# Optimization experiments

Hardware: AMD Instinct MI355X
Metric: run time of the kernel (lower is better)

Reference implementation:

```python
import jax, jax.numpy as jnp
import numpy as np


def setup_inputs() -> dict:
    key = jax.random.key(0)
    k1, k2 = jax.random.split(key)
    B, T_enc, T_dec, D = 8, 2048, 2048, 128
    encoder_hidden_states = jax.random.normal(k1, (B, T_enc, D), dtype=jnp.float32)
    decoder_hidden_states = jax.random.normal(k2, (B, T_dec, D), dtype=jnp.float32)
    return {"encoder_hidden_states": encoder_hidden_states,
            "decoder_hidden_states": decoder_hidden_states}


def reference(encoder_hidden_states, decoder_hidden_states):
    # dot_product[b,q,k] = dec[b,q,:] . enc[b,k,:]
    dot_product = jnp.einsum("bqd,bkd->bqk", decoder_hidden_states, encoder_hidden_states)
    # attn_scores[b,q,d] = sum_k dot_product[b,q,k] * enc[b,k,d]
    # (the torch code materializes the 4D broadcast; this is the same math as a bmm)
    attn_scores = jnp.einsum("bqk,bkd->bqd", dot_product, encoder_hidden_states)
    return attn_scores
```

## Files before the change

### kernel.cpp

```cpp
#include <hip/hip_runtime.h>

#define BB 8
#define TT 2048
#define DD 128
#define CH 32
#define GT_STRIDE 72

typedef __attribute__((ext_vector_type(8))) short bf16x8;
typedef __attribute__((ext_vector_type(4))) float f32x4;
typedef unsigned short u16;

static __device__ __forceinline__ float bf2f(u16 u) {
    union { unsigned int i; float f; } v; v.i = ((unsigned int)u) << 16; return v.f;
}
static __device__ __forceinline__ u16 f2bf(float f) {
    union { float f; unsigned int i; } v; v.f = f;
    unsigned int x = v.i;
    return (u16)((x + 0x7FFFu + ((x >> 16) & 1u)) >> 16);
}

__global__ __launch_bounds__(256, 1) void gram_mfma(const float* __restrict__ enc,
                                                    u16* __restrict__ P) {
    const int b     = blockIdx.y;
    const int chunk = blockIdx.x;
    const int t     = threadIdx.x;

    __shared__ __align__(16) u16 Gt[DD * GT_STRIDE];

    const int d  = t & 127;
    const int kh = t >> 7;
    const int wave = t >> 6, lane = t & 63, quad = lane >> 4, ln = lane & 15;

    f32x4 acc[2][8];
    #pragma unroll
    for (int mi = 0; mi < 2; ++mi)
        #pragma unroll
        for (int nt = 0; nt < 8; ++nt) acc[mi][nt] = (f32x4){0.f, 0.f, 0.f, 0.f};

    const float* src = enc + ((size_t)b * TT + (size_t)chunk * 64) * DD;
    #pragma unroll
    for (int a = 0; a < 8; ++a) {
        const int k4 = a * 2 + kh;
        u16 o[4];
        #pragma unroll
        for (int i = 0; i < 4; ++i)
            o[i] = f2bf(src[(k4 * 4 + i) * DD + d]);
        *(ushort4*)&Gt[d * GT_STRIDE + k4 * 4] = *(const ushort4*)o;
    }
    __syncthreads();

    bf16x8 afrag[2][2];
    #pragma unroll
    for (int mi = 0; mi < 2; ++mi)
        #pragma unroll
        for (int ks = 0; ks < 2; ++ks)
            afrag[mi][ks] = *(const bf16x8*)&Gt[((wave * 2 + mi) * 16 + ln) * GT_STRIDE
                                                + ks * 32 + quad * 8];
    #pragma unroll
    for (int ks = 0; ks < 2; ++ks) {
        #pragma unroll
        for (int nt = 0; nt < 8; ++nt) {
            const bf16x8 bfrag = *(const bf16x8*)&Gt[(nt * 16 + ln) * GT_STRIDE
                                                     + ks * 32 + quad * 8];
            #pragma unroll
            for (int mi = 0; mi < 2; ++mi)
                acc[mi][nt] = __builtin_amdgcn_mfma_f32_16x16x32_bf16(
                    afrag[mi][ks], bfrag, acc[mi][nt], 0, 0, 0);
        }
    }

    u16* Pb = P + ((size_t)chunk * BB + b) * (DD * DD);
    const int off = ln * 16 + (quad >> 1) * 8 + (quad & 1) * 4;
    #pragma unroll
    for (int mi = 0; mi < 2; ++mi) {
        #pragma unroll
        for (int nt = 0; nt < 8; ++nt) {
            u16 o[4];
            #pragma unroll
            for (int r = 0; r < 4; ++r) o[r] = f2bf(acc[mi][nt][r]);
            const int tile = (wave * 2 + mi) * 8 + nt;
            *(ushort4*)&Pb[tile * 256 + off] = *(const ushort4*)o;
        }
    }
}

__global__ __launch_bounds__(128) void gram_reduce(const u16* __restrict__ P,
                                                   u16* __restrict__ Gw) {
    const int g = blockIdx.x * 128 + threadIdx.x;
    const ushort4* Pu = (const ushort4*)P;
    const int stride = BB * DD * DD / 4;
    float sx = 0.f, sy = 0.f, sz = 0.f, sw = 0.f;
    #pragma unroll
    for (int c = 0; c < CH; ++c) {
        const ushort4 v = Pu[(size_t)c * stride + g];
        sx += bf2f(v.x); sy += bf2f(v.y); sz += bf2f(v.z); sw += bf2f(v.w);
    }
    ushort4 o; o.x = f2bf(sx); o.y = f2bf(sy); o.z = f2bf(sz); o.w = f2bf(sw);
    ((ushort4*)Gw)[g] = o;
}

__global__ __launch_bounds__(256, 1) void apply_mfma(const float* __restrict__ dec,
                                                     const u16* __restrict__ Gw,
                                                     float* __restrict__ out) {
    const int b     = blockIdx.y;
    const int chunk = blockIdx.x;
    const int t     = threadIdx.x;

    __shared__ __align__(16) u16 Gs[DD * DD];

    const int wave = t >> 6, lane = t & 63, quad = lane >> 4, ln = lane & 15;
    const int qt = wave * 16;

    const float* drow = dec + ((size_t)b * TT + (size_t)chunk * 64 + qt + ln) * DD
                        + quad * 8;
    float4 dv[4][2];
    #pragma unroll
    for (int ks = 0; ks < 4; ++ks) {
        dv[ks][0] = *(const float4*)(drow + ks * 32);
        dv[ks][1] = *(const float4*)(drow + ks * 32 + 4);
    }

    const uint4* gsrc = (const uint4*)(Gw + (size_t)b * DD * DD);
    #pragma unroll
    for (int i = 0; i < 8; ++i)
        ((uint4*)Gs)[i * 256 + t] = gsrc[i * 256 + t];

    bf16x8 afrag[4];
    #pragma unroll
    for (int ks = 0; ks < 4; ++ks) {
        union { u16 o[8]; bf16x8 v; } u;
        u.o[0] = f2bf(dv[ks][0].x); u.o[1] = f2bf(dv[ks][0].y);
        u.o[2] = f2bf(dv[ks][0].z); u.o[3] = f2bf(dv[ks][0].w);
        u.o[4] = f2bf(dv[ks][1].x); u.o[5] = f2bf(dv[ks][1].y);
        u.o[6] = f2bf(dv[ks][1].z); u.o[7] = f2bf(dv[ks][1].w);
        afrag[ks] = u.v;
    }
    __syncthreads();

    f32x4 acc[8];
    #pragma unroll
    for (int dt = 0; dt < 8; ++dt) acc[dt] = (f32x4){0.f, 0.f, 0.f, 0.f};

    #pragma unroll
    for (int ks = 0; ks < 4; ++ks) {
        const int mtk  = ks * 2 + (quad >> 1);
        const int boff = ln * 16 + (quad & 1) * 8;
        #pragma unroll
        for (int dt = 0; dt < 8; ++dt) {
            const bf16x8 bb = *(const bf16x8*)&Gs[(mtk * 8 + dt) * 256 + boff];
            acc[dt] = __builtin_amdgcn_mfma_f32_16x16x32_bf16(afrag[ks], bb, acc[dt], 0, 0, 0);
        }
    }

    float* ob = out + ((size_t)b * TT + (size_t)chunk * 64) * DD;
    #pragma unroll
    for (int dt = 0; dt < 8; ++dt) {
        const int dcol = dt * 16 + ln;
        #pragma unroll
        for (int r = 0; r < 4; ++r) {
            const int q = qt + quad * 4 + r;
            ob[q * DD + dcol] = acc[dt][r];
        }
    }
}

extern "C" void kernel_launch(void* const* d_in, const int* in_sizes, int n_in,
                              void* d_out, int out_size, void* d_ws, size_t ws_size,
                              hipStream_t stream) {
    const float* enc = (const float*)d_in[0];
    const float* dec = (const float*)d_in[1];
    float* out = (float*)d_out;

    u16* P  = (u16*)d_ws;
    u16* Gw = (u16*)((char*)d_ws + (size_t)CH * BB * DD * DD * sizeof(u16));

    gram_mfma<<<dim3(CH, BB), 256, 0, stream>>>(enc, P);
    gram_reduce<<<BB * DD * DD / 4 / 128, 128, 0, stream>>>(P, Gw);
    apply_mfma<<<dim3(TT / 64, BB), 256, 0, stream>>>(dec, Gw, out);
}
```

Before: 75.71 us.

## Fuse gram, reduce and apply kernels into one cooperative kernel with grid syncs

Merges the three launches (per-chunk Gram MFMA, cross-chunk reduction, apply MFMA) into a single cooperative kernel separated by grid-wide barriers, reusing one shared buffer. This removes inter-kernel launch gaps and tail effects. In exchange it adds two grid synchronizations and forces all blocks to be co-resident, and the reduce phase now runs with half its threads idle.

```diff
diff --git a/kernel.cpp b/kernel.cpp
--- a/kernel.cpp
+++ b/kernel.cpp
@@ -1,4 +1,7 @@
 #include <hip/hip_runtime.h>
+#include <hip/hip_cooperative_groups.h>
+
+namespace cg = cooperative_groups;
 
 #define BB 8
 #define TT 2048
@@ -19,147 +22,151 @@
     return (u16)((x + 0x7FFFu + ((x >> 16) & 1u)) >> 16);
 }
 
-__global__ __launch_bounds__(256, 1) void gram_mfma(const float* __restrict__ enc,
-                                                    u16* __restrict__ P) {
-    const int b     = blockIdx.y;
-    const int chunk = blockIdx.x;
-    const int t     = threadIdx.x;
+__global__ __launch_bounds__(256, 1) void fused_luong(const float* __restrict__ enc,
+                                                      const float* __restrict__ dec,
+                                                      u16* __restrict__ P,
+                                                      u16* __restrict__ Gw,
+                                                      float* __restrict__ out) {
+    const int bid  = blockIdx.x;
+    const int t    = threadIdx.x;
+    const int wave = t >> 6, lane = t & 63, quad = lane >> 4, ln = lane & 15;
+    const int chunk = bid & (CH - 1);
+    const int b     = bid >> 5;
 
-    __shared__ __align__(16) u16 Gt[DD * GT_STRIDE];
+    __shared__ __align__(16) u16 smem[DD * DD];
 
-    const int d  = t & 127;
-    const int kh = t >> 7;
-    const int wave = t >> 6, lane = t & 63, quad = lane >> 4, ln = lane & 15;
+    {
+        const int d  = t & 127;
+        const int kh = t >> 7;
 
-    f32x4 acc[2][8];
-    #pragma unroll
-    for (int mi = 0; mi < 2; ++mi)
+        f32x4 acc[2][8];
         #pragma unroll
-        for (int nt = 0; nt < 8; ++nt) acc[mi][nt] = (f32x4){0.f, 0.f, 0.f, 0.f};
+        for (int mi = 0; mi < 2; ++mi)
+            #pragma unroll
+            for (int nt = 0; nt < 8; ++nt) acc[mi][nt] = (f32x4){0.f, 0.f, 0.f, 0.f};
 
-    const float* src = enc + ((size_t)b * TT + (size_t)chunk * 64) * DD;
-    #pragma unroll
-    for (int a = 0; a < 8; ++a) {
-        const int k4 = a * 2 + kh;
-        u16 o[4];
+        const float* src = enc + ((size_t)b * TT + (size_t)chunk * 64) * DD;
         #pragma unroll
-        for (int i = 0; i < 4; ++i)
-            o[i] = f2bf(src[(k4 * 4 + i) * DD + d]);
-        *(ushort4*)&Gt[d * GT_STRIDE + k4 * 4] = *(const ushort4*)o;
-    }
-    __syncthreads();
+        for (int a = 0; a < 8; ++a) {
+            const int k4 = a * 2 + kh;
+            u16 o[4];
+            #pragma unroll
+            for (int i = 0; i < 4; ++i)
+                o[i] = f2bf(src[(k4 * 4 + i) * DD + d]);
+            *(ushort4*)&smem[d * GT_STRIDE + k4 * 4] = *(const ushort4*)o;
+        }
+        __syncthreads();
 
-    bf16x8 afrag[2][2];
-    #pragma unroll
-    for (int mi = 0; mi < 2; ++mi)
+        bf16x8 afrag[2][2];
         #pragma unroll
-        for (int ks = 0; ks < 2; ++ks)
-            afrag[mi][ks] = *(const bf16x8*)&Gt[((wave * 2 + mi) * 16 + ln) * GT_STRIDE
-                                                + ks * 32 + quad * 8];
-    #pragma unroll
-    for (int ks = 0; ks < 2; ++ks) {
+        for (int mi = 0; mi < 2; ++mi)
+            #pragma unroll
+            for (int ks = 0; ks < 2; ++ks)
+                afrag[mi][ks] = *(const bf16x8*)&smem[((wave * 2 + mi) * 16 + ln) * GT_STRIDE
+                                                      + ks * 32 + quad * 8];
         #pragma unroll
-        for (int nt = 0; nt < 8; ++nt) {
-            const bf16x8 bfrag = *(const bf16x8*)&Gt[(nt * 16 + ln) * GT_STRIDE
-                                                     + ks * 32 + quad * 8];
+        for (int ks = 0; ks < 2; ++ks) {
             #pragma unroll
-            for (int mi = 0; mi < 2; ++mi)
-                acc[mi][nt] = __builtin_amdgcn_mfma_f32_16x16x32_bf16(
-                    afrag[mi][ks], bfrag, acc[mi][nt], 0, 0, 0);
+            for (int nt = 0; nt < 8; ++nt) {
+                const bf16x8 bfrag = *(const bf16x8*)&smem[(nt * 16 + ln) * GT_STRIDE
+                                                           + ks * 32 + quad * 8];
+                #pragma unroll
+                for (int mi = 0; mi < 2; ++mi)
+                    acc[mi][nt] = __builtin_amdgcn_mfma_f32_16x16x32_bf16(
+                        afrag[mi][ks], bfrag, acc[mi][nt], 0, 0, 0);
+            }
+        }
+
+        u16* Pb = P + ((size_t)chunk * BB + b) * (DD * DD);
+        const int off = ln * 16 + (quad >> 1) * 8 + (quad & 1) * 4;
+        #pragma unroll
+        for (int mi = 0; mi < 2; ++mi) {
+            #pragma unroll
+            for (int nt = 0; nt < 8; ++nt) {
+                u16 o[4];
+                #pragma unroll
+                for (int r = 0; r < 4; ++r) o[r] = f2bf(acc[mi][nt][r]);
+                const int tile = (wave * 2 + mi) * 8 + nt;
+                *(ushort4*)&Pb[tile * 256 + off] = *(const ushort4*)o;
+            }
         }
     }
 
-    u16* Pb = P + ((size_t)chunk * BB + b) * (DD * DD);
-    const int off = ln * 16 + (quad >> 1) * 8 + (quad & 1) * 4;
-    #pragma unroll
-    for (int mi = 0; mi < 2; ++mi) {
-        #pragma unroll
-        for (int nt = 0; nt < 8; ++nt) {
-            u16 o[4];
+    __threadfence();
+    cg::this_grid().sync();
+
+    {
+        const int g = bid * 256 + t;
+        if (g < BB * DD * DD / 4) {
+            const ushort4* Pu = (const ushort4*)P;
+            const int stride = BB * DD * DD / 4;
+            float sx = 0.f, sy = 0.f, sz = 0.f, sw = 0.f;
             #pragma unroll
-            for (int r = 0; r < 4; ++r) o[r] = f2bf(acc[mi][nt][r]);
-            const int tile = (wave * 2 + mi) * 8 + nt;
-            *(ushort4*)&Pb[tile * 256 + off] = *(const ushort4*)o;
-        }
-    }
-}
-
-__global__ __launch_bounds__(128) void gram_reduce(const u16* __restrict__ P,
-                                                   u16* __restrict__ Gw) {
-    const int g = blockIdx.x * 128 + threadIdx.x;
-    const ushort4* Pu = (const ushort4*)P;
-    const int stride = BB * DD * DD / 4;
-    float sx = 0.f, sy = 0.f, sz = 0.f, sw = 0.f;
-    #pragma unroll
-    for (int c = 0; c < CH; ++c) {
-        const ushort4 v = Pu[(size_t)c * stride + g];
-        sx += bf2f(v.x); sy += bf2f(v.y); sz += bf2f(v.z); sw += bf2f(v.w);
-    }
-    ushort4 o; o.x = f2bf(sx); o.y = f2bf(sy); o.z = f2bf(sz); o.w = f2bf(sw);
-    ((ushort4*)Gw)[g] = o;
-}
-
-__global__ __launch_bounds__(256, 1) void apply_mfma(const float* __restrict__ dec,
-                                                     const u16* __restrict__ Gw,
-                                                     float* __restrict__ out) {
-    const int b     = blockIdx.y;
-    const int chunk = blockIdx.x;
-    const int t     = threadIdx.x;
-
-    __shared__ __align__(16) u16 Gs[DD * DD];
-
-    const int wave = t >> 6, lane = t & 63, quad = lane >> 4, ln = lane & 15;
-    const int qt = wave * 16;
-
-    const float* drow = dec + ((size_t)b * TT + (size_t)chunk * 64 + qt + ln) * DD
-                        + quad * 8;
-    float4 dv[4][2];
-    #pragma unroll
-    for (int ks = 0; ks < 4; ++ks) {
-        dv[ks][0] = *(const float4*)(drow + ks * 32);
-        dv[ks][1] = *(const float4*)(drow + ks * 32 + 4);
-    }
-
-    const uint4* gsrc = (const uint4*)(Gw + (size_t)b * DD * DD);
-    #pragma unroll
-    for (int i = 0; i < 8; ++i)
-        ((uint4*)Gs)[i * 256 + t] = gsrc[i * 256 + t];
-
-    bf16x8 afrag[4];
-    #pragma unroll
-    for (int ks = 0; ks < 4; ++ks) {
-        union { u16 o[8]; bf16x8 v; } u;
-        u.o[0] = f2bf(dv[ks][0].x); u.o[1] = f2bf(dv[ks][0].y);
-        u.o[2] = f2bf(dv[ks][0].z); u.o[3] = f2bf(dv[ks][0].w);
-        u.o[4] = f2bf(dv[ks][1].x); u.o[5] = f2bf(dv[ks][1].y);
-        u.o[6] = f2bf(dv[ks][1].z); u.o[7] = f2bf(dv[ks][1].w);
-        afrag[ks] = u.v;
-    }
-    __syncthreads();
-
-    f32x4 acc[8];
-    #pragma unroll
-    for (int dt = 0; dt < 8; ++dt) acc[dt] = (f32x4){0.f, 0.f, 0.f, 0.f};
-
-    #pragma unroll
-    for (int ks = 0; ks < 4; ++ks) {
-        const int mtk  = ks * 2 + (quad >> 1);
-        const int boff = ln * 16 + (quad & 1) * 8;
-        #pragma unroll
-        for (int dt = 0; dt < 8; ++dt) {
-            const bf16x8 bb = *(const bf16x8*)&Gs[(mtk * 8 + dt) * 256 + boff];
-            acc[dt] = __builtin_amdgcn_mfma_f32_16x16x32_bf16(afrag[ks], bb, acc[dt], 0, 0, 0);
+            for (int c = 0; c < CH; ++c) {
+                const ushort4 v = Pu[(size_t)c * stride + g];
+                sx += bf2f(v.x); sy += bf2f(v.y); sz += bf2f(v.z); sw += bf2f(v.w);
+            }
+            ushort4 o; o.x = f2bf(sx); o.y = f2bf(sy); o.z = f2bf(sz); o.w = f2bf(sw);
+            ((ushort4*)Gw)[g] = o;
         }
     }
 
-    float* ob = out + ((size_t)b * TT + (size_t)chunk * 64) * DD;
-    #pragma unroll
-    for (int dt = 0; dt < 8; ++dt) {
-        const int dcol = dt * 16 + ln;
+    __threadfence();
+    cg::this_grid().sync();
+
+    {
+        const int qt = wave * 16;
+
+        const float* drow = dec + ((size_t)b * TT + (size_t)chunk * 64 + qt + ln) * DD
+                            + quad * 8;
+        float4 dv[4][2];
         #pragma unroll
-        for (int r = 0; r < 4; ++r) {
-            const int q = qt + quad * 4 + r;
-            ob[q * DD + dcol] = acc[dt][r];
+        for (int ks = 0; ks < 4; ++ks) {
+            dv[ks][0] = *(const float4*)(drow + ks * 32);
+            dv[ks][1] = *(const float4*)(drow + ks * 32 + 4);
+        }
+
+        const uint4* gsrc = (const uint4*)(Gw + (size_t)b * DD * DD);
+        #pragma unroll
+        for (int i = 0; i < 8; ++i)
+            ((uint4*)smem)[i * 256 + t] = gsrc[i * 256 + t];
+
+        bf16x8 afrag[4];
+        #pragma unroll
+        for (int ks = 0; ks < 4; ++ks) {
+            union { u16 o[8]; bf16x8 v; } u;
+            u.o[0] = f2bf(dv[ks][0].x); u.o[1] = f2bf(dv[ks][0].y);
+            u.o[2] = f2bf(dv[ks][0].z); u.o[3] = f2bf(dv[ks][0].w);
+            u.o[4] = f2bf(dv[ks][1].x); u.o[5] = f2bf(dv[ks][1].y);
+            u.o[6] = f2bf(dv[ks][1].z); u.o[7] = f2bf(dv[ks][1].w);
+            afrag[ks] = u.v;
+        }
+        __syncthreads();
+
+        f32x4 acc[8];
+        #pragma unroll
+        for (int dt = 0; dt < 8; ++dt) acc[dt] = (f32x4){0.f, 0.f, 0.f, 0.f};
+
+        #pragma unroll
+        for (int ks = 0; ks < 4; ++ks) {
+            const int mtk  = ks * 2 + (quad >> 1);
+            const int boff = ln * 16 + (quad & 1) * 8;
+            #pragma unroll
+            for (int dt = 0; dt < 8; ++dt) {
+                const bf16x8 bb = *(const bf16x8*)&smem[(mtk * 8 + dt) * 256 + boff];
+                acc[dt] = __builtin_amdgcn_mfma_f32_16x16x32_bf16(afrag[ks], bb, acc[dt], 0, 0, 0);
+            }
+        }
+
+        float* ob = out + ((size_t)b * TT + (size_t)chunk * 64) * DD;
+        #pragma unroll
+        for (int dt = 0; dt < 8; ++dt) {
+            const int dcol = dt * 16 + ln;
+            #pragma unroll
+            for (int r = 0; r < 4; ++r) {
+                const int q = qt + quad * 4 + r;
+                ob[q * DD + dcol] = acc[dt][r];
+            }
         }
     }
 }
@@ -174,7 +181,7 @@
     u16* P  = (u16*)d_ws;
     u16* Gw = (u16*)((char*)d_ws + (size_t)CH * BB * DD * DD * sizeof(u16));
 
-    gram_mfma<<<dim3(CH, BB), 256, 0, stream>>>(enc, P);
-    gram_reduce<<<BB * DD * DD / 4 / 128, 128, 0, stream>>>(P, Gw);
-    apply_mfma<<<dim3(TT / 64, BB), 256, 0, stream>>>(dec, Gw, out);
+    void* args[] = {(void*)&enc, (void*)&dec, (void*)&P, (void*)&Gw, (void*)&out};
+    hipLaunchCooperativeKernel((void*)fused_luong, dim3(CH * BB), dim3(256),
+                               args, 0, stream);
 }
```

Result: slower. 182.8 us (+141.4%).

## Fuse Gram, reduce and apply into one kernel with per-block Gram recompute

Applied to the files above, without the earlier changes.

Replaces the three-kernel pipeline (per-chunk partial Gram, global reduction, apply) with a single kernel. Each block now loops over all 32 encoder chunks of its batch and accumulates the full 128x128 Gram matrix in registers. It then writes the result to shared memory and multiplies its decoder tile against it. This removes the workspace round-trip and two launches, and keeps Gram accumulation in fp32 instead of summing bf16 partials. The cost is that every block redundantly recomputes the whole Gram, so the encoder is read 32x more often and there is a long serial load/MFMA loop per block.

```diff
diff --git a/kernel.cpp b/kernel.cpp
--- a/kernel.cpp
+++ b/kernel.cpp
@@ -3,33 +3,47 @@
 #define BB 8
 #define TT 2048
 #define DD 128
-#define CH 32
+#define NCH 32
 #define GT_STRIDE 72
 
 typedef __attribute__((ext_vector_type(8))) short bf16x8;
 typedef __attribute__((ext_vector_type(4))) float f32x4;
 typedef unsigned short u16;
 
-static __device__ __forceinline__ float bf2f(u16 u) {
-    union { unsigned int i; float f; } v; v.i = ((unsigned int)u) << 16; return v.f;
-}
 static __device__ __forceinline__ u16 f2bf(float f) {
     union { float f; unsigned int i; } v; v.f = f;
     unsigned int x = v.i;
     return (u16)((x + 0x7FFFu + ((x >> 16) & 1u)) >> 16);
 }
 
-__global__ __launch_bounds__(256, 1) void gram_mfma(const float* __restrict__ enc,
-                                                    u16* __restrict__ P) {
-    const int b     = blockIdx.y;
-    const int chunk = blockIdx.x;
+__global__ __launch_bounds__(256, 1) void luong_fused(const float* __restrict__ enc,
+                                                      const float* __restrict__ dec,
+                                                      float* __restrict__ out) {
+    const int bid   = blockIdx.x;
+    const int b     = bid & 7;
+    const int chunk = bid >> 3;
     const int t     = threadIdx.x;
+    const int wave  = t >> 6, lane = t & 63, quad = lane >> 4, ln = lane & 15;
 
-    __shared__ __align__(16) u16 Gt[DD * GT_STRIDE];
+    __shared__ __align__(16) u16 Gt[2][DD * GT_STRIDE];
+    __shared__ __align__(16) u16 Gs[DD * DD];
+
+    const int qt = wave * 16;
+    const float* drow = dec + ((size_t)b * TT + (size_t)chunk * 64 + qt + ln) * DD
+                        + quad * 8;
+    bf16x8 afrag[4];
+    #pragma unroll
+    for (int ks = 0; ks < 4; ++ks) {
+        const float4 d0 = *(const float4*)(drow + ks * 32);
+        const float4 d1 = *(const float4*)(drow + ks * 32 + 4);
+        union { u16 o[8]; bf16x8 v; } u;
+        u.o[0] = f2bf(d0.x); u.o[1] = f2bf(d0.y); u.o[2] = f2bf(d0.z); u.o[3] = f2bf(d0.w);
+        u.o[4] = f2bf(d1.x); u.o[5] = f2bf(d1.y); u.o[6] = f2bf(d1.z); u.o[7] = f2bf(d1.w);
+        afrag[ks] = u.v;
+    }
 
     const int d  = t & 127;
     const int kh = t >> 7;
-    const int wave = t >> 6, lane = t & 63, quad = lane >> 4, ln = lane & 15;
 
     f32x4 acc[2][8];
     #pragma unroll
@@ -37,39 +51,41 @@
         #pragma unroll
         for (int nt = 0; nt < 8; ++nt) acc[mi][nt] = (f32x4){0.f, 0.f, 0.f, 0.f};
 
-    const float* src = enc + ((size_t)b * TT + (size_t)chunk * 64) * DD;
-    #pragma unroll
-    for (int a = 0; a < 8; ++a) {
-        const int k4 = a * 2 + kh;
-        u16 o[4];
+    for (int kc = 0; kc < NCH; ++kc) {
+        u16* gt = Gt[kc & 1];
+        const float* src = enc + ((size_t)b * TT + (size_t)kc * 64) * DD;
         #pragma unroll
-        for (int i = 0; i < 4; ++i)
-            o[i] = f2bf(src[(k4 * 4 + i) * DD + d]);
-        *(ushort4*)&Gt[d * GT_STRIDE + k4 * 4] = *(const ushort4*)o;
-    }
-    __syncthreads();
+        for (int a = 0; a < 8; ++a) {
+            const int k4 = a * 2 + kh;
+            u16 o[4];
+            #pragma unroll
+            for (int i = 0; i < 4; ++i)
+                o[i] = f2bf(src[(k4 * 4 + i) * DD + d]);
+            *(ushort4*)&gt[d * GT_STRIDE + k4 * 4] = *(const ushort4*)o;
+        }
+        __syncthreads();
 
-    bf16x8 afrag[2][2];
-    #pragma unroll
-    for (int mi = 0; mi < 2; ++mi)
+        bf16x8 ga[2][2];
         #pragma unroll
-        for (int ks = 0; ks < 2; ++ks)
-            afrag[mi][ks] = *(const bf16x8*)&Gt[((wave * 2 + mi) * 16 + ln) * GT_STRIDE
-                                                + ks * 32 + quad * 8];
-    #pragma unroll
-    for (int ks = 0; ks < 2; ++ks) {
+        for (int mi = 0; mi < 2; ++mi)
+            #pragma unroll
+            for (int ks = 0; ks < 2; ++ks)
+                ga[mi][ks] = *(const bf16x8*)&gt[((wave * 2 + mi) * 16 + ln) * GT_STRIDE
+                                                 + ks * 32 + quad * 8];
         #pragma unroll
-        for (int nt = 0; nt < 8; ++nt) {
-            const bf16x8 bfrag = *(const bf16x8*)&Gt[(nt * 16 + ln) * GT_STRIDE
-                                                     + ks * 32 + quad * 8];
+        for (int ks = 0; ks < 2; ++ks) {
             #pragma unroll
-            for (int mi = 0; mi < 2; ++mi)
-                acc[mi][nt] = __builtin_amdgcn_mfma_f32_16x16x32_bf16(
-                    afrag[mi][ks], bfrag, acc[mi][nt], 0, 0, 0);
+            for (int nt = 0; nt < 8; ++nt) {
+                const bf16x8 gb = *(const bf16x8*)&gt[(nt * 16 + ln) * GT_STRIDE
+                                                      + ks * 32 + quad * 8];
+                #pragma unroll
+                for (int mi = 0; mi < 2; ++mi)
+                    acc[mi][nt] = __builtin_amdgcn_mfma_f32_16x16x32_bf16(
+                        ga[mi][ks], gb, acc[mi][nt], 0, 0, 0);
+            }
         }
     }
 
-    u16* Pb = P + ((size_t)chunk * BB + b) * (DD * DD);
     const int off = ln * 16 + (quad >> 1) * 8 + (quad & 1) * 4;
     #pragma unroll
     for (int mi = 0; mi < 2; ++mi) {
@@ -79,67 +95,14 @@
             #pragma unroll
             for (int r = 0; r < 4; ++r) o[r] = f2bf(acc[mi][nt][r]);
             const int tile = (wave * 2 + mi) * 8 + nt;
-            *(ushort4*)&Pb[tile * 256 + off] = *(const ushort4*)o;
+            *(ushort4*)&Gs[tile * 256 + off] = *(const ushort4*)o;
         }
-    }
-}
-
-__global__ __launch_bounds__(128) void gram_reduce(const u16* __restrict__ P,
-                                                   u16* __restrict__ Gw) {
-    const int g = blockIdx.x * 128 + threadIdx.x;
-    const ushort4* Pu = (const ushort4*)P;
-    const int stride = BB * DD * DD / 4;
-    float sx = 0.f, sy = 0.f, sz = 0.f, sw = 0.f;
-    #pragma unroll
-    for (int c = 0; c < CH; ++c) {
-        const ushort4 v = Pu[(size_t)c * stride + g];
-        sx += bf2f(v.x); sy += bf2f(v.y); sz += bf2f(v.z); sw += bf2f(v.w);
-    }
-    ushort4 o; o.x = f2bf(sx); o.y = f2bf(sy); o.z = f2bf(sz); o.w = f2bf(sw);
-    ((ushort4*)Gw)[g] = o;
-}
-
-__global__ __launch_bounds__(256, 1) void apply_mfma(const float* __restrict__ dec,
-                                                     const u16* __restrict__ Gw,
-                                                     float* __restrict__ out) {
-    const int b     = blockIdx.y;
-    const int chunk = blockIdx.x;
-    const int t     = threadIdx.x;
-
-    __shared__ __align__(16) u16 Gs[DD * DD];
-
-    const int wave = t >> 6, lane = t & 63, quad = lane >> 4, ln = lane & 15;
-    const int qt = wave * 16;
-
-    const float* drow = dec + ((size_t)b * TT + (size_t)chunk * 64 + qt + ln) * DD
-                        + quad * 8;
-    float4 dv[4][2];
-    #pragma unroll
-    for (int ks = 0; ks < 4; ++ks) {
-        dv[ks][0] = *(const float4*)(drow + ks * 32);
-        dv[ks][1] = *(const float4*)(drow + ks * 32 + 4);
-    }
-
-    const uint4* gsrc = (const uint4*)(Gw + (size_t)b * DD * DD);
-    #pragma unroll
-    for (int i = 0; i < 8; ++i)
-        ((uint4*)Gs)[i * 256 + t] = gsrc[i * 256 + t];
-
-    bf16x8 afrag[4];
-    #pragma unroll
-    for (int ks = 0; ks < 4; ++ks) {
-        union { u16 o[8]; bf16x8 v; } u;
-        u.o[0] = f2bf(dv[ks][0].x); u.o[1] = f2bf(dv[ks][0].y);
-        u.o[2] = f2bf(dv[ks][0].z); u.o[3] = f2bf(dv[ks][0].w);
-        u.o[4] = f2bf(dv[ks][1].x); u.o[5] = f2bf(dv[ks][1].y);
-        u.o[6] = f2bf(dv[ks][1].z); u.o[7] = f2bf(dv[ks][1].w);
-        afrag[ks] = u.v;
     }
     __syncthreads();
 
-    f32x4 acc[8];
+    f32x4 oacc[8];
     #pragma unroll
-    for (int dt = 0; dt < 8; ++dt) acc[dt] = (f32x4){0.f, 0.f, 0.f, 0.f};
+    for (int dt = 0; dt < 8; ++dt) oacc[dt] = (f32x4){0.f, 0.f, 0.f, 0.f};
 
     #pragma unroll
     for (int ks = 0; ks < 4; ++ks) {
@@ -147,8 +110,8 @@
         const int boff = ln * 16 + (quad & 1) * 8;
         #pragma unroll
         for (int dt = 0; dt < 8; ++dt) {
-            const bf16x8 bb = *(const bf16x8*)&Gs[(mtk * 8 + dt) * 256 + boff];
-            acc[dt] = __builtin_amdgcn_mfma_f32_16x16x32_bf16(afrag[ks], bb, acc[dt], 0, 0, 0);
+            const bf16x8 gb = *(const bf16x8*)&Gs[(mtk * 8 + dt) * 256 + boff];
+            oacc[dt] = __builtin_amdgcn_mfma_f32_16x16x32_bf16(afrag[ks], gb, oacc[dt], 0, 0, 0);
         }
     }
 
@@ -159,7 +122,7 @@
         #pragma unroll
         for (int r = 0; r < 4; ++r) {
             const int q = qt + quad * 4 + r;
-            ob[q * DD + dcol] = acc[dt][r];
+            ob[q * DD + dcol] = oacc[dt][r];
         }
     }
 }
@@ -170,11 +133,7 @@
     const float* enc = (const float*)d_in[0];
     const float* dec = (const float*)d_in[1];
     float* out = (float*)d_out;
+    (void)d_ws; (void)ws_size;
 
-    u16* P  = (u16*)d_ws;
-    u16* Gw = (u16*)((char*)d_ws + (size_t)CH * BB * DD * DD * sizeof(u16));
-
-    gram_mfma<<<dim3(CH, BB), 256, 0, stream>>>(enc, P);
-    gram_reduce<<<BB * DD * DD / 4 / 128, 128, 0, stream>>>(P, Gw);
-    apply_mfma<<<dim3(TT / 64, BB), 256, 0, stream>>>(dec, Gw, out);
+    luong_fused<<<dim3(BB * NCH), 256, 0, stream>>>(enc, dec, out);
 }
```

Measured after the change: 165.3 us. 2.18x slower.
